# Kernel tuning notes

Hardware: AMD Instinct MI355X
Metric: run time of the kernel (lower is better)

## Reference

```python
import jax, jax.numpy as jnp
import numpy as np

K = 3          # s_kernel_size = max_graph_distance + 1
C_OUT = 128    # out_channel


def setup_inputs() -> dict:
    key = jax.random.key(0)
    k1, k2, k3, k4 = jax.random.split(key, 4)
    N, C_IN, T, V = 64, 64, 256, 25
    x = jax.random.normal(k1, (N, C_IN, T, V), dtype=jnp.float32)
    # 1x1 Conv2d(in_channel, out_channel*K) weight/bias
    W = jax.random.normal(k2, (K * C_OUT, C_IN), dtype=jnp.float32) * 0.05
    b = jax.random.normal(k3, (K * C_OUT,), dtype=jnp.float32) * 0.05
    # fixed adjacency stack (non-trainable buffer-like param)
    A = jax.random.uniform(k4, (K, V, V), dtype=jnp.float32)
    edge = jnp.ones((K, V, V), dtype=jnp.float32)       # init ones_like(A)
    adaptive_A = jnp.zeros((K, V, V), dtype=jnp.float32)  # init zeros_like(A)
    return {"x": x, "W": W, "b": b, "A": A, "edge": edge, "adaptive_A": adaptive_A}


def reference(x, W, b, A, edge, adaptive_A):
    n, c_in, t, v = x.shape
    # 1x1 conv == per-pixel GEMM over channel dim: (n,c,t,v) -> (n, K*C_OUT, t, v)
    y = jnp.einsum('nctv,oc->notv', x, W) + b[None, :, None, None]
    y = y.reshape(n, K, C_OUT, t, v)                 # (n, k, c, t, v)
    effective_A = A * edge + adaptive_A              # (k, v, w)
    out = jnp.einsum('nkctv,kvw->nctw', y, effective_A)
    return out
```

## Files before the change

### kernel.cpp

```cpp
#include <hip/hip_runtime.h>
#include <hip/hip_bf16.h>

typedef __bf16 bf16x8 __attribute__((ext_vector_type(8)));
typedef float floatx4 __attribute__((ext_vector_type(4)));

#define ROWK 200
#define ZROWS 112

__global__ void sgc_prep(const float* __restrict__ W, const float* __restrict__ b,
                         const float* __restrict__ A, const float* __restrict__ edge,
                         const float* __restrict__ adA,
                         __hip_bfloat16* __restrict__ Wp, float* __restrict__ effAT,
                         float* __restrict__ bias2) {
  int tid = blockIdx.x * blockDim.x + threadIdx.x;
  int nthr = gridDim.x * blockDim.x;
  for (int i = tid; i < 24576; i += nthr) {
    int c = i / 192; int r = i - c * 192; int k = r >> 6; int ci = r & 63;
    Wp[i] = __float2bfloat16(W[(k * 128 + c) * 64 + ci]);
  }
  for (int i = tid; i < 2100; i += nthr) {
    int kw = i / 28; int v = i - kw * 28;
    int k = kw / 25; int w = kw - k * 25;
    float val = 0.f;
    if (v < 25) {
      int idx = (k * 25 + v) * 25 + w;
      val = A[idx] * edge[idx] + adA[idx];
    }
    effAT[i] = val;
  }
  for (int i = tid; i < 3200; i += nthr) {
    int c = i / 25; int w = i - c * 25;
    float s = 0.f;
    for (int k = 0; k < 3; k++) {
      float sv = 0.f;
      for (int v = 0; v < 25; v++) {
        int idx = (k * 25 + v) * 25 + w;
        sv += A[idx] * edge[idx] + adA[idx];
      }
      s += b[k * 128 + c] * sv;
    }
    bias2[i] = s;
  }
}

__global__ __launch_bounds__(256, 2)
void sgc_main(const float* __restrict__ x,
              const __hip_bfloat16* __restrict__ Wp,
              const float* __restrict__ effAT,
              const float* __restrict__ bias2,
              float* __restrict__ out) {
  __shared__ __hip_bfloat16 zt[ZROWS * ROWK];
  const int tid = threadIdx.x;
  const int lane = tid & 63;
  const int wv = tid >> 6;
  const int blk = blockIdx.x;

  const int col = lane & 15;
  const int quad = lane >> 4;
  const int kb = quad * 8;

  bf16x8 afr[2][6];
#pragma unroll
  for (int mtl = 0; mtl < 2; mtl++) {
    int c = (2 * wv + mtl) * 16 + col;
    const __hip_bfloat16* wrow = Wp + c * 192;
#pragma unroll
    for (int ks = 0; ks < 6; ks++)
      afr[mtl][ks] = *(const bf16x8*)(wrow + ks * 32 + kb);
  }

  floatx4 acc[2][7];
#pragma unroll
  for (int nt = 0; nt < 7; nt++) {
    int nn = nt * 16 + col;
    int p = (nn * 41) >> 10;
    int w = nn - p * 25;
#pragma unroll
    for (int mtl = 0; mtl < 2; mtl++) {
      int c0 = (2 * wv + mtl) * 16 + quad * 4;
#pragma unroll
      for (int r = 0; r < 4; r++)
        acc[mtl][nt][r] = bias2[(c0 + r) * 25 + w];
    }
  }

  {
    const int p = wv, ci = lane;
    const int g = blk * 4 + p;
    const int n = g >> 8, t = g & 255;
    const float* xrow = x + ((size_t)(n * 64 + ci) * 256 + t) * 25;
    float xr[25];
#pragma unroll
    for (int v = 0; v < 25; v++) xr[v] = xrow[v];
    for (int kw = 0; kw < 75; kw++) {
      const float* colp = effAT + kw * 28;
      float a = 0.f;
#pragma unroll
      for (int v = 0; v < 25; v++) a = fmaf(xr[v], colp[v], a);
      int k = (kw < 25) ? 0 : ((kw < 50) ? 1 : 2);
      int w = kw - k * 25;
      zt[(p * 25 + w) * ROWK + k * 64 + ci] = __float2bfloat16(a);
    }
  }
  __syncthreads();

  const __hip_bfloat16* ztp = zt;
#pragma unroll
  for (int ks = 0; ks < 6; ks++) {
    bf16x8 bfr[7];
#pragma unroll
    for (int nt = 0; nt < 7; nt++)
      bfr[nt] = *(const bf16x8*)(ztp + (nt * 16 + col) * ROWK + ks * 32 + kb);
#pragma unroll
    for (int nt = 0; nt < 7; nt++) {
      acc[0][nt] = __builtin_amdgcn_mfma_f32_16x16x32_bf16(afr[0][ks], bfr[nt], acc[0][nt], 0, 0, 0);
      acc[1][nt] = __builtin_amdgcn_mfma_f32_16x16x32_bf16(afr[1][ks], bfr[nt], acc[1][nt], 0, 0, 0);
    }
  }

#pragma unroll
  for (int nt = 0; nt < 7; nt++) {
    int nn = nt * 16 + col;
    if (nn >= 100) continue;
    int p = (nn * 41) >> 10;
    int w = nn - p * 25;
    int g = blk * 4 + p;
    int n = g >> 8, t = g & 255;
#pragma unroll
    for (int mtl = 0; mtl < 2; mtl++) {
      int c0 = (2 * wv + mtl) * 16 + quad * 4;
      size_t base = ((size_t)(n * 128 + c0) * 256 + t) * 25 + w;
#pragma unroll
      for (int r = 0; r < 4; r++)
        out[base + (size_t)r * 6400] = acc[mtl][nt][r];
    }
  }
}

extern "C" void kernel_launch(void* const* d_in, const int* in_sizes, int n_in,
                              void* d_out, int out_size, void* d_ws, size_t ws_size,
                              hipStream_t stream) {
  const float* x    = (const float*)d_in[0];
  const float* W    = (const float*)d_in[1];
  const float* b    = (const float*)d_in[2];
  const float* A    = (const float*)d_in[3];
  const float* edge = (const float*)d_in[4];
  const float* adA  = (const float*)d_in[5];
  float* out = (float*)d_out;

  char* ws = (char*)d_ws;
  __hip_bfloat16* Wp = (__hip_bfloat16*)ws;
  float* effAT = (float*)(ws + 49152);
  float* bias2 = (float*)(ws + 57600);

  sgc_prep<<<64, 256, 0, stream>>>(W, b, A, edge, adA, Wp, effAT, bias2);
  sgc_main<<<4096, 256, 0, stream>>>(x, Wp, effAT, bias2, out);
}
```

Before: 395.0 us.

## Compute adjacency contraction with bf16 MFMA instead of scalar FMA loop

New measurement: 380.5 us. 3.7% less time.

```diff
diff --git a/kernel.cpp b/kernel.cpp
--- a/kernel.cpp
+++ b/kernel.cpp
@@ -2,7 +2,9 @@
 #include <hip/hip_bf16.h>
 
 typedef __bf16 bf16x8 __attribute__((ext_vector_type(8)));
+typedef __bf16 bf16x4 __attribute__((ext_vector_type(4)));
 typedef float floatx4 __attribute__((ext_vector_type(4)));
+typedef float floatx4u __attribute__((ext_vector_type(4), aligned(4)));
 
 #define ROWK 200
 #define ZROWS 112
@@ -10,7 +12,7 @@
 __global__ void sgc_prep(const float* __restrict__ W, const float* __restrict__ b,
                          const float* __restrict__ A, const float* __restrict__ edge,
                          const float* __restrict__ adA,
-                         __hip_bfloat16* __restrict__ Wp, float* __restrict__ effAT,
+                         __hip_bfloat16* __restrict__ Wp, __hip_bfloat16* __restrict__ effAB,
                          float* __restrict__ bias2) {
   int tid = blockIdx.x * blockDim.x + threadIdx.x;
   int nthr = gridDim.x * blockDim.x;
@@ -18,15 +20,15 @@
     int c = i / 192; int r = i - c * 192; int k = r >> 6; int ci = r & 63;
     Wp[i] = __float2bfloat16(W[(k * 128 + c) * 64 + ci]);
   }
-  for (int i = tid; i < 2100; i += nthr) {
-    int kw = i / 28; int v = i - kw * 28;
-    int k = kw / 25; int w = kw - k * 25;
+  for (int i = tid; i < 2560; i += nthr) {
+    int n = i >> 5; int v = i & 31;
     float val = 0.f;
-    if (v < 25) {
+    if (n < 75 && v < 25) {
+      int k = n / 25; int w = n - k * 25;
       int idx = (k * 25 + v) * 25 + w;
       val = A[idx] * edge[idx] + adA[idx];
     }
-    effAT[i] = val;
+    effAB[i] = __float2bfloat16(val);
   }
   for (int i = tid; i < 3200; i += nthr) {
     int c = i / 25; int w = i - c * 25;
@@ -43,10 +45,10 @@
   }
 }
 
-__global__ __launch_bounds__(256, 2)
+__global__ __launch_bounds__(256, 3)
 void sgc_main(const float* __restrict__ x,
               const __hip_bfloat16* __restrict__ Wp,
-              const float* __restrict__ effAT,
+              const __hip_bfloat16* __restrict__ effAB,
               const float* __restrict__ bias2,
               float* __restrict__ out) {
   __shared__ __hip_bfloat16 zt[ZROWS * ROWK];
@@ -58,6 +60,50 @@
   const int col = lane & 15;
   const int quad = lane >> 4;
   const int kb = quad * 8;
+
+  bf16x8 bA[5];
+#pragma unroll
+  for (int nt = 0; nt < 5; nt++)
+    bA[nt] = *(const bf16x8*)(effAB + (nt * 16 + col) * 32 + kb);
+
+  {
+    const int g = blk * 4 + wv;
+    const int n0 = g >> 8, t = g & 255;
+    const float* xbase = x + (size_t)(n0 * 64) * 6400 + (size_t)t * 25;
+#pragma unroll
+    for (int mt = 0; mt < 4; mt++) {
+      const int ci = mt * 16 + col;
+      const float* xr = xbase + (size_t)ci * 6400;
+      bf16x8 xa;
+      if (quad < 3) {
+        floatx4u a = *(const floatx4u*)(xr + kb);
+        floatx4u c = *(const floatx4u*)(xr + kb + 4);
+        xa = (bf16x8){(__bf16)a.x, (__bf16)a.y, (__bf16)a.z, (__bf16)a.w,
+                      (__bf16)c.x, (__bf16)c.y, (__bf16)c.z, (__bf16)c.w};
+      } else {
+        float v24 = xr[24];
+        xa = (bf16x8){(__bf16)v24, (__bf16)0.f, (__bf16)0.f, (__bf16)0.f,
+                      (__bf16)0.f, (__bf16)0.f, (__bf16)0.f, (__bf16)0.f};
+      }
+      floatx4 zacc[5];
+#pragma unroll
+      for (int nt = 0; nt < 5; nt++) {
+        zacc[nt] = (floatx4){0.f, 0.f, 0.f, 0.f};
+        zacc[nt] = __builtin_amdgcn_mfma_f32_16x16x32_bf16(xa, bA[nt], zacc[nt], 0, 0, 0);
+      }
+#pragma unroll
+      for (int nt = 0; nt < 5; nt++) {
+        int nn = nt * 16 + col;
+        if (nn < 75) {
+          int k = (nn * 41) >> 10;
+          int w = nn - k * 25;
+          bf16x4 zb = (bf16x4){(__bf16)zacc[nt][0], (__bf16)zacc[nt][1],
+                               (__bf16)zacc[nt][2], (__bf16)zacc[nt][3]};
+          *(bf16x4*)(zt + (wv * 25 + w) * ROWK + k * 64 + mt * 16 + quad * 4) = zb;
+        }
+      }
+    }
+  }
 
   bf16x8 afr[2][6];
 #pragma unroll
@@ -84,24 +130,6 @@
     }
   }
 
-  {
-    const int p = wv, ci = lane;
-    const int g = blk * 4 + p;
-    const int n = g >> 8, t = g & 255;
-    const float* xrow = x + ((size_t)(n * 64 + ci) * 256 + t) * 25;
-    float xr[25];
-#pragma unroll
-    for (int v = 0; v < 25; v++) xr[v] = xrow[v];
-    for (int kw = 0; kw < 75; kw++) {
-      const float* colp = effAT + kw * 28;
-      float a = 0.f;
-#pragma unroll
-      for (int v = 0; v < 25; v++) a = fmaf(xr[v], colp[v], a);
-      int k = (kw < 25) ? 0 : ((kw < 50) ? 1 : 2);
-      int w = kw - k * 25;
-      zt[(p * 25 + w) * ROWK + k * 64 + ci] = __float2bfloat16(a);
-    }
-  }
   __syncthreads();
 
   const __hip_bfloat16* ztp = zt;
@@ -149,10 +177,10 @@
   float* out = (float*)d_out;
 
   char* ws = (char*)d_ws;
-  __hip_bfloat16* Wp = (__hip_bfloat16*)ws;
-  float* effAT = (float*)(ws + 49152);
-  float* bias2 = (float*)(ws + 57600);
+  __hip_bfloat16* Wp    = (__hip_bfloat16*)ws;
+  __hip_bfloat16* effAB = (__hip_bfloat16*)(ws + 49152);
+  float* bias2          = (float*)(ws + 54272);
 
-  sgc_prep<<<64, 256, 0, stream>>>(W, b, A, edge, adA, Wp, effAT, bias2);
-  sgc_main<<<4096, 256, 0, stream>>>(x, Wp, effAT, bias2, out);
+  sgc_prep<<<64, 256, 0, stream>>>(W, b, A, edge, adA, Wp, effAB, bias2);
+  sgc_main<<<4096, 256, 0, stream>>>(x, Wp, effAB, bias2, out);
 }
```
